# Kernel tuning notes

Hardware: AMD Instinct MI355X
Metric: run time of the kernel (lower is better)

Reference implementation:

```python
import jax, jax.numpy as jnp
import numpy as np

HIDDEN = 2048
N_HEADS = 32
N_KV_HEADS = 8
HEAD_DIM = HIDDEN // N_HEADS  # 64
N_REP = N_HEADS // N_KV_HEADS  # 4
ROPE_THETA = 10000.0


def setup_inputs() -> dict:
    key = jax.random.key(0)
    ks = jax.random.split(key, 5)
    b, s = 2, 2048
    x = jax.random.normal(ks[0], (b, s, HIDDEN), dtype=jnp.float32)
    position_ids = jnp.arange(b * s, dtype=jnp.int32).reshape(b, s)
    sc = 1.0 / np.sqrt(HIDDEN)
    Wq = jax.random.normal(ks[1], (HIDDEN, HIDDEN), dtype=jnp.float32) * sc
    Wk = jax.random.normal(ks[2], (HIDDEN, N_KV_HEADS * HEAD_DIM), dtype=jnp.float32) * sc
    Wv = jax.random.normal(ks[3], (HIDDEN, N_KV_HEADS * HEAD_DIM), dtype=jnp.float32) * sc
    Wo = jax.random.normal(ks[4], (HIDDEN, HIDDEN), dtype=jnp.float32) * sc
    return {"input_ids": x, "Wq": Wq, "Wk": Wk, "Wv": Wv, "Wo": Wo,
            "position_ids": position_ids}


def _rope_cos_sin(position_ids, dtype):
    # inv_freq: [head_dim/2]
    inv_freq = 1.0 / (ROPE_THETA ** (jnp.arange(0, HEAD_DIM, 2, dtype=jnp.float32) / HEAD_DIM))
    freqs = position_ids.astype(jnp.float32)[..., None] * inv_freq  # [b, s, d/2]
    emb = jnp.concatenate([freqs, freqs], axis=-1)  # [b, s, d]
    return emb.astype(dtype), None  # placeholder, replaced below


def _rotate_half(x):
    x1, x2 = jnp.split(x, 2, axis=-1)
    return jnp.concatenate([-x2, x1], axis=-1)


def reference(input_ids, Wq, Wk, Wv, Wo, position_ids):
    b, s, _ = input_ids.shape
    q = (input_ids @ Wq).reshape(b, s, N_HEADS, HEAD_DIM).transpose(0, 2, 1, 3)      # [b,H,s,d]
    k = (input_ids @ Wk).reshape(b, s, N_KV_HEADS, HEAD_DIM).transpose(0, 2, 1, 3)   # [b,Hkv,s,d]
    v = (input_ids @ Wv).reshape(b, s, N_KV_HEADS, HEAD_DIM).transpose(0, 2, 1, 3)

    # RoPE
    inv_freq = 1.0 / (ROPE_THETA ** (jnp.arange(0, HEAD_DIM, 2, dtype=jnp.float32) / HEAD_DIM))
    freqs = position_ids.astype(jnp.float32)[..., None] * inv_freq  # [b,s,d/2]
    emb = jnp.concatenate([freqs, freqs], axis=-1)                   # [b,s,d]
    cos = jnp.cos(emb).astype(input_ids.dtype)[:, None, :, :]        # [b,1,s,d]
    sin = jnp.sin(emb).astype(input_ids.dtype)[:, None, :, :]
    q = q * cos + _rotate_half(q) * sin
    k = k * cos + _rotate_half(k) * sin

    # repeat_kv: [b,Hkv,s,d] -> [b,H,s,d]
    k = jnp.repeat(k, N_REP, axis=1)
    v = jnp.repeat(v, N_REP, axis=1)

    # causal SDPA
    scale = 1.0 / np.sqrt(HEAD_DIM)
    scores = jnp.einsum('bhqd,bhkd->bhqk', q, k) * scale
    causal = jnp.tril(jnp.ones((s, s), dtype=bool))
    scores = jnp.where(causal, scores, jnp.finfo(scores.dtype).min)
    attn = jax.nn.softmax(scores, axis=-1)
    out = jnp.einsum('bhqk,bhkd->bhqd', attn, v)                     # [b,H,s,d]
    out = out.transpose(0, 2, 1, 3).reshape(b, s, HIDDEN)
    return out @ Wo
```

## Files before the change

### kernel.cpp

```cpp
#include <hip/hip_runtime.h>
#include <hip/hip_bf16.h>

#define HIDDEN 2048
#define NHEADS 32
#define NKVH   8
#define HD     64
#define BATCH  2
#define SEQ    2048
#define ROWS   (BATCH * SEQ)
#define NQKV   3072
#define KCOL   2048
#define VCOL   2560

typedef __bf16 bf16x8 __attribute__((ext_vector_type(8)));
typedef __bf16 bf16x4 __attribute__((ext_vector_type(4)));
typedef float  f32x4  __attribute__((ext_vector_type(4)));
typedef short  s16x4  __attribute__((ext_vector_type(4)));
typedef short  s16x8  __attribute__((ext_vector_type(8)));

__device__ __forceinline__ void gl2lds16(const void* g, void* l) {
  __builtin_amdgcn_global_load_lds(
      (const __attribute__((address_space(1))) void*)g,
      (__attribute__((address_space(3))) void*)l, 16, 0, 0);
}

__device__ __forceinline__ short f2bs(float f) {
  __bf16 h = (__bf16)f;
  return __builtin_bit_cast(short, h);
}

__device__ __forceinline__ float fexp2(float x) {
#if __has_builtin(__builtin_amdgcn_exp2f)
  return __builtin_amdgcn_exp2f(x);
#else
  return exp2f(x);
#endif
}

__device__ __forceinline__ f32x4 mfma16(s16x4 a, s16x4 b, f32x4 c) {
#if __has_builtin(__builtin_amdgcn_mfma_f32_16x16x16bf16_1k)
  return __builtin_amdgcn_mfma_f32_16x16x16bf16_1k(a, b, c, 0, 0, 0);
#else
  s16x8 a8 = __builtin_shufflevector(a, (s16x4){0,0,0,0}, 0,1,2,3,4,5,6,7);
  s16x8 b8 = __builtin_shufflevector(b, (s16x4){0,0,0,0}, 0,1,2,3,4,5,6,7);
  a8[4]=0;a8[5]=0;a8[6]=0;a8[7]=0; b8[4]=0;b8[5]=0;b8[6]=0;b8[7]=0;
  return __builtin_amdgcn_mfma_f32_16x16x32_bf16(
      __builtin_bit_cast(bf16x8, a8), __builtin_bit_cast(bf16x8, b8), c, 0, 0, 0);
#endif
}

__global__ void prep(const float* __restrict__ Wq, const float* __restrict__ Wk,
                     const float* __restrict__ Wv, const float* __restrict__ Wo,
                     const float* __restrict__ x,
                     __bf16* __restrict__ dstW, __bf16* __restrict__ Xb) {
  __shared__ __bf16 tile[32][33];
  int bid = blockIdx.x, tid = threadIdx.x;
  if (bid < 10240) {
    int n0 = (bid % 160) * 32, k0 = (bid / 160) * 32;
    int tx = tid & 31, ty = tid >> 5;
    const float* src;
    int N, c0;
    if (n0 < 2048)      { src = Wq; N = 2048; c0 = n0; }
    else if (n0 < 2560) { src = Wk; N = 512;  c0 = n0 - 2048; }
    else if (n0 < 3072) { src = Wv; N = 512;  c0 = n0 - 2560; }
    else                { src = Wo; N = 2048; c0 = n0 - 3072; }
#pragma unroll
    for (int i = 0; i < 32; i += 8)
      tile[ty + i][tx] = (__bf16)src[(size_t)(k0 + ty + i) * N + (c0 + tx)];
    __syncthreads();
#pragma unroll
    for (int i = 0; i < 32; i += 8)
      dstW[(size_t)(n0 + ty + i) * HIDDEN + (k0 + tx)] = tile[tx][ty + i];
  } else {
    size_t i = (size_t)(bid - 10240) * 256 + tid;
    const float4* s = (const float4*)(x + i * 16);
    float4 a = s[0], b = s[1], c = s[2], d = s[3];
    bf16x8 o0, o1;
    o0[0] = (__bf16)a.x; o0[1] = (__bf16)a.y; o0[2] = (__bf16)a.z; o0[3] = (__bf16)a.w;
    o0[4] = (__bf16)b.x; o0[5] = (__bf16)b.y; o0[6] = (__bf16)b.z; o0[7] = (__bf16)b.w;
    o1[0] = (__bf16)c.x; o1[1] = (__bf16)c.y; o1[2] = (__bf16)c.z; o1[3] = (__bf16)c.w;
    o1[4] = (__bf16)d.x; o1[5] = (__bf16)d.y; o1[6] = (__bf16)d.z; o1[7] = (__bf16)d.w;
    *(bf16x8*)(Xb + i * 16)     = o0;
    *(bf16x8*)(Xb + i * 16 + 8) = o1;
  }
}

template <typename OutT, bool ROPE>
__launch_bounds__(256, 2)
__global__ void gemm_bt(const __bf16* __restrict__ A, const __bf16* __restrict__ Bt,
                        OutT* __restrict__ C, int M, int N, int K,
                        const int* __restrict__ pos_ids, __bf16* __restrict__ Vt) {
  __shared__ __bf16 As[2][128 * 32];
  __shared__ __bf16 Bs[2][128 * 32];
  int id = blockIdx.x;
  int bm = (id & 7) * 4 + ((id >> 3) & 3);
  int bn = id >> 5;
  int t = threadIdx.x;
  int wave = t >> 6, lane = t & 63, l16 = lane & 15, quad = lane >> 4;
  int wm = (wave >> 1) * 64, wn = (wave & 1) * 64;

  f32x4 acc[4][4] = {};

  int arow = t >> 2;
  int ac   = (t & 3) * 8;
  const __bf16* Ag = A  + (size_t)(bm * 128 + arow) * K + ac;
  const __bf16* Bg = Bt + (size_t)(bn * 128 + arow) * K + ac;
  int woff = wave * 512;

  for (int k0 = 0; k0 < K; k0 += 64) {
    __syncthreads();
    gl2lds16(Ag + k0,                      &As[0][woff]);
    gl2lds16(Ag + (size_t)64 * K + k0,      &As[0][2048 + woff]);
    gl2lds16(Ag + k0 + 32,                 &As[1][woff]);
    gl2lds16(Ag + (size_t)64 * K + k0 + 32, &As[1][2048 + woff]);
    gl2lds16(Bg + k0,                      &Bs[0][woff]);
    gl2lds16(Bg + (size_t)64 * K + k0,      &Bs[0][2048 + woff]);
    gl2lds16(Bg + k0 + 32,                 &Bs[1][woff]);
    gl2lds16(Bg + (size_t)64 * K + k0 + 32, &Bs[1][2048 + woff]);
    __syncthreads();

#pragma unroll
    for (int ks = 0; ks < 2; ++ks) {
      bf16x8 af[4], bfr[4];
#pragma unroll
      for (int i = 0; i < 4; ++i) {
        af[i]  = *(const bf16x8*)(&As[ks][(wm + i * 16 + l16) * 32 + quad * 8]);
        bfr[i] = *(const bf16x8*)(&Bs[ks][(wn + i * 16 + l16) * 32 + quad * 8]);
      }
#pragma unroll
      for (int i = 0; i < 4; ++i)
#pragma unroll
        for (int j = 0; j < 4; ++j)
          acc[i][j] = __builtin_amdgcn_mfma_f32_16x16x32_bf16(af[i], bfr[j], acc[i][j], 0, 0, 0);
    }
  }

  if (ROPE) {
    int headidx = bn * 2 + (wn >> 6);
    if (headidx >= 40) {
#pragma unroll
      for (int i = 0; i < 4; ++i) {
        int srow = bm * 128 + wm + i * 16 + quad * 4;
        int b = srow >> 11, s = srow & 2047;
#pragma unroll
        for (int j = 0; j < 4; ++j) {
          int vcol = bn * 128 + wn + j * 16 + l16 - VCOL;
          int hk = vcol >> 6, d = vcol & 63;
          bf16x4 w;
#pragma unroll
          for (int r = 0; r < 4; ++r) w[r] = (__bf16)acc[i][j][r];
          *(bf16x4*)(Vt + ((size_t)(b * NKVH + hk) * HD + d) * SEQ + s) = w;
        }
      }
      return;
    }
    float invrev0 = __expf(-(float)l16 * 0.28782313662425574f) * 0.15915494309189535f;
    float invrev1 = __expf(-(float)(l16 + 16) * 0.28782313662425574f) * 0.15915494309189535f;
#pragma unroll
    for (int i = 0; i < 4; ++i)
#pragma unroll
      for (int r = 0; r < 4; ++r) {
        int gr = bm * 128 + wm + i * 16 + quad * 4 + r;
        float pos = (float)pos_ids[gr];
        float rv0 = pos * invrev0; rv0 -= floorf(rv0);
        float rv1 = pos * invrev1; rv1 -= floorf(rv1);
        float a0 = rv0 * 6.283185307179586f, a1 = rv1 * 6.283185307179586f;
        float s0 = __sinf(a0), c0 = __cosf(a0);
        float s1 = __sinf(a1), c1 = __cosf(a1);
        float x0 = acc[i][0][r], x2 = acc[i][2][r];
        acc[i][0][r] = x0 * c0 - x2 * s0;
        acc[i][2][r] = x2 * c0 + x0 * s0;
        float x1 = acc[i][1][r], x3 = acc[i][3][r];
        acc[i][1][r] = x1 * c1 - x3 * s1;
        acc[i][3][r] = x3 * c1 + x1 * s1;
      }
  }

#pragma unroll
  for (int i = 0; i < 4; ++i)
#pragma unroll
    for (int j = 0; j < 4; ++j)
#pragma unroll
      for (int r = 0; r < 4; ++r)
        C[(size_t)(bm * 128 + wm + i * 16 + quad * 4 + r) * N +
          (bn * 128 + wn + j * 16 + l16)] = (OutT)acc[i][j][r];
}

__launch_bounds__(256, 4)
__global__ void flash_attn(const __bf16* __restrict__ QKV, const __bf16* __restrict__ Vt,
                           __bf16* __restrict__ O) {
  int wgid = blockIdx.x + 64 * (blockIdx.y + 8 * (int)blockIdx.z);
  int swz  = (wgid & 7) * 128 + (wgid >> 3);
  int b  = swz >> 9;
  int hk = (swz >> 6) & 7;
  int bx = swz & 63;
  int p  = bx >> 2;
  int np = 31 - p;
  int h  = hk * 4 + (bx & 3);

  int t = threadIdx.x;
  int wave = t >> 6, lane = t & 63, l16 = lane & 15, quad = lane >> 4;

  __shared__ __bf16 Ks[2][2][64 * 32];
  __shared__ __bf16 Vs[2][4096];

  const __bf16* Kbase = QKV + (size_t)(b * SEQ) * NQKV + KCOL + hk * HD;
  const __bf16* VtB   = Vt + (size_t)(b * NKVH + hk) * HD * SEQ;

  int kr = wave * 16 + (lane >> 2);
  int kc = (lane & 3) * 8;
  int vd = wave * 16 + (lane >> 2);
  int vsc = (lane & 3) * 16;
  int vs4w = (lane & 3) * 4;

  const s16x4 vones = { (short)0x3F80, (short)0x3F80, (short)0x3F80, (short)0x3F80 };

  bf16x8 qfrag[2][2];
#pragma unroll
  for (int qi = 0; qi < 2; ++qi) {
    int qt = qi ? np : p;
    const __bf16* qp = QKV + (size_t)(b * SEQ + qt * 64 + wave * 16 + l16) * NQKV
                     + h * HD + quad * 8;
    bf16x8 q0 = *(const bf16x8*)qp;
    bf16x8 q1 = *(const bf16x8*)(qp + 32);
#pragma unroll
    for (int e = 0; e < 8; ++e) {
      qfrag[qi][0][e] = (__bf16)((float)q0[e] * 0.18033688011112042f);
      qfrag[qi][1][e] = (__bf16)((float)q1[e] * 0.18033688011112042f);
    }
  }

  f32x4 lacc[2] = { {0.f,0.f,0.f,0.f}, {0.f,0.f,0.f,0.f} };
  f32x4 oacc[2][4];
#pragma unroll
  for (int qi = 0; qi < 2; ++qi)
#pragma unroll
    for (int dt = 0; dt < 4; ++dt) oacc[qi][dt] = (f32x4){0.f, 0.f, 0.f, 0.f};

  {
    const __bf16* kp = Kbase + (size_t)kr * NQKV + kc;
    gl2lds16(kp,      &Ks[0][0][wave * 512]);
    gl2lds16(kp + 32, &Ks[0][1][wave * 512]);
    const __bf16* vp = VtB + (size_t)vd * SEQ + vsc;
    s16x8 v0 = __builtin_bit_cast(s16x8, *(const bf16x8*)vp);
    s16x8 v1 = __builtin_bit_cast(s16x8, *(const bf16x8*)(vp + 8));
    *(s16x4*)(&Vs[0][(vs4w + 0) * 256 + vd * 4]) = __builtin_shufflevector(v0, v0, 0, 1, 2, 3);
    *(s16x4*)(&Vs[0][(vs4w + 1) * 256 + vd * 4]) = __builtin_shufflevector(v0, v0, 4, 5, 6, 7);
    *(s16x4*)(&Vs[0][(vs4w + 2) * 256 + vd * 4]) = __builtin_shufflevector(v1, v1, 0, 1, 2, 3);
    *(s16x4*)(&Vs[0][(vs4w + 3) * 256 + vd * 4]) = __builtin_shufflevector(v1, v1, 4, 5, 6, 7);
  }

  for (int kt = 0; kt <= np; ++kt) {
    int buf = kt & 1;
    __syncthreads();

    bool pre = (kt < np);
    s16x8 pv0, pv1;
    if (pre) {
      const __bf16* kp = Kbase + (size_t)((kt + 1) * 64 + kr) * NQKV + kc;
      gl2lds16(kp,      &Ks[buf ^ 1][0][wave * 512]);
      gl2lds16(kp + 32, &Ks[buf ^ 1][1][wave * 512]);
      const __bf16* vp = VtB + (size_t)vd * SEQ + (kt + 1) * 64 + vsc;
      pv0 = __builtin_bit_cast(s16x8, *(const bf16x8*)vp);
      pv1 = __builtin_bit_cast(s16x8, *(const bf16x8*)(vp + 8));
    }

    bool a0 = (kt <= p);

    f32x4 s0[4], s1[4];
#pragma unroll
    for (int nt = 0; nt < 4; ++nt) {
      s0[nt] = (f32x4){0.f, 0.f, 0.f, 0.f};
      s1[nt] = (f32x4){0.f, 0.f, 0.f, 0.f};
    }
#pragma unroll
    for (int ks = 0; ks < 2; ++ks) {
      bf16x8 kf[4];
#pragma unroll
      for (int nt = 0; nt < 4; ++nt)
        kf[nt] = *(const bf16x8*)(&Ks[buf][ks][(nt * 16 + l16) * 32 + quad * 8]);
      __builtin_amdgcn_s_setprio(1);
#pragma unroll
      for (int nt = 0; nt < 4; ++nt)
        s1[nt] = __builtin_amdgcn_mfma_f32_16x16x32_bf16(kf[nt], qfrag[1][ks], s1[nt], 0, 0, 0);
      if (a0) {
#pragma unroll
        for (int nt = 0; nt < 4; ++nt)
          s0[nt] = __builtin_amdgcn_mfma_f32_16x16x32_bf16(kf[nt], qfrag[0][ks], s0[nt], 0, 0, 0);
      }
      __builtin_amdgcn_s_setprio(0);
    }

    s16x4 af0[4], af1[4];
    {
      int qg = wave * 16 + l16;
      if (kt == np) {
#pragma unroll
        for (int nt = 0; nt < 4; ++nt)
#pragma unroll
          for (int r = 0; r < 4; ++r) {
            int kg = nt * 16 + quad * 4 + r;
            af1[nt][r] = f2bs(fexp2((kg > qg) ? -1e30f : s1[nt][r]));
          }
      } else {
#pragma unroll
        for (int nt = 0; nt < 4; ++nt)
#pragma unroll
          for (int r = 0; r < 4; ++r)
            af1[nt][r] = f2bs(fexp2(s1[nt][r]));
      }
      if (a0) {
        if (kt == p) {
#pragma unroll
          for (int nt = 0; nt < 4; ++nt)
#pragma unroll
            for (int r = 0; r < 4; ++r) {
              int kg = nt * 16 + quad * 4 + r;
              af0[nt][r] = f2bs(fexp2((kg > qg) ? -1e30f : s0[nt][r]));
            }
        } else {
#pragma unroll
          for (int nt = 0; nt < 4; ++nt)
#pragma unroll
            for (int r = 0; r < 4; ++r)
              af0[nt][r] = f2bs(fexp2(s0[nt][r]));
        }
      }
    }

#pragma unroll
    for (int nt = 0; nt < 4; ++nt) {
      s16x4 vf[4];
#pragma unroll
      for (int dt = 0; dt < 4; ++dt)
        vf[dt] = *(const s16x4*)(&Vs[buf][(nt * 4 + quad) * 256 + (dt * 16 + l16) * 4]);
      __builtin_amdgcn_s_setprio(1);
#pragma unroll
      for (int dt = 0; dt < 4; ++dt)
        oacc[1][dt] = mfma16(af1[nt], vf[dt], oacc[1][dt]);
      lacc[1] = mfma16(af1[nt], vones, lacc[1]);
      if (a0) {
#pragma unroll
        for (int dt = 0; dt < 4; ++dt)
          oacc[0][dt] = mfma16(af0[nt], vf[dt], oacc[0][dt]);
        lacc[0] = mfma16(af0[nt], vones, lacc[0]);
      }
      __builtin_amdgcn_s_setprio(0);
    }

    if (pre) {
      *(s16x4*)(&Vs[buf ^ 1][(vs4w + 0) * 256 + vd * 4]) = __builtin_shufflevector(pv0, pv0, 0, 1, 2, 3);
      *(s16x4*)(&Vs[buf ^ 1][(vs4w + 1) * 256 + vd * 4]) = __builtin_shufflevector(pv0, pv0, 4, 5, 6, 7);
      *(s16x4*)(&Vs[buf ^ 1][(vs4w + 2) * 256 + vd * 4]) = __builtin_shufflevector(pv1, pv1, 0, 1, 2, 3);
      *(s16x4*)(&Vs[buf ^ 1][(vs4w + 3) * 256 + vd * 4]) = __builtin_shufflevector(pv1, pv1, 4, 5, 6, 7);
    }
  }

#pragma unroll
  for (int qi = 0; qi < 2; ++qi) {
    int qt = qi ? np : p;
#pragma unroll
    for (int r = 0; r < 4; ++r) {
      float inv = 1.0f / lacc[qi][r];
#pragma unroll
      for (int dt = 0; dt < 4; ++dt) {
        float o = oacc[qi][dt][r] * inv;
        O[(size_t)(b * SEQ + qt * 64 + wave * 16 + quad * 4 + r) * HIDDEN +
          h * HD + dt * 16 + l16] = (__bf16)o;
      }
    }
  }
}

extern "C" void kernel_launch(void* const* d_in, const int* in_sizes, int n_in,
                              void* d_out, int out_size, void* d_ws, size_t ws_size,
                              hipStream_t stream) {
  const float* x  = (const float*)d_in[0];
  const float* Wq = (const float*)d_in[1];
  const float* Wk = (const float*)d_in[2];
  const float* Wv = (const float*)d_in[3];
  const float* Wo = (const float*)d_in[4];
  const int* pos  = (const int*)d_in[5];

  __bf16* Wqkvt = (__bf16*)d_ws;
  __bf16* Wot   = Wqkvt + (size_t)NQKV * HIDDEN;
  __bf16* Xb    = Wot + (size_t)HIDDEN * HIDDEN;
  __bf16* QKV   = Xb + (size_t)ROWS * HIDDEN;
  __bf16* Oat   = QKV + (size_t)ROWS * NQKV;
  __bf16* Vt    = Xb;

  prep<<<dim3(12288), 256, 0, stream>>>(Wq, Wk, Wv, Wo, x, Wqkvt, Xb);

  gemm_bt<__bf16, true><<<dim3(768), 256, 0, stream>>>(
      Xb, Wqkvt, QKV, ROWS, NQKV, HIDDEN, pos, Vt);

  flash_attn<<<dim3(64, NKVH, BATCH), 256, 0, stream>>>(QKV, Vt, Oat);

  gemm_bt<float, false><<<dim3(512), 256, 0, stream>>>(
      Oat, Wot, (float*)d_out, ROWS, HIDDEN, HIDDEN, nullptr, nullptr);
}
```

Baseline: 285.9 us.

## Pair adjacent query tiles per workgroup with balanced XCD head mapping

```diff
diff --git a/kernel.cpp b/kernel.cpp
--- a/kernel.cpp
+++ b/kernel.cpp
@@ -190,13 +190,18 @@
 __global__ void flash_attn(const __bf16* __restrict__ QKV, const __bf16* __restrict__ Vt,
                            __bf16* __restrict__ O) {
   int wgid = blockIdx.x + 64 * (blockIdx.y + 8 * (int)blockIdx.z);
-  int swz  = (wgid & 7) * 128 + (wgid >> 3);
-  int b  = swz >> 9;
-  int hk = (swz >> 6) & 7;
-  int bx = swz & 63;
-  int p  = bx >> 2;
-  int np = 31 - p;
-  int h  = hk * 4 + (bx & 3);
+  int xcd  = wgid & 7;
+  int j    = wgid >> 3;
+  int G    = j >> 6;
+  int gid  = xcd * 2 + G;
+  int b    = gid >> 3;
+  int hk   = gid & 7;
+  int r    = j & 63;
+  int b0   = r & 1, b5 = (r >> 5) & 1;
+  int h    = hk * 4 + b0 + 2 * b5;
+  int M0   = (r >> 1) & 15;
+  int M    = (b0 ^ b5) ? (15 - M0) : M0;
+  int NT   = 2 * M + 2;
 
   int t = threadIdx.x;
   int wave = t >> 6, lane = t & 63, l16 = lane & 15, quad = lane >> 4;
@@ -209,7 +214,7 @@
 
   int kr = wave * 16 + (lane >> 2);
   int kc = (lane & 3) * 8;
-  int vd = wave * 16 + (lane >> 2);
+  int vd = kr;
   int vsc = (lane & 3) * 16;
   int vs4w = (lane & 3) * 4;
 
@@ -218,8 +223,7 @@
   bf16x8 qfrag[2][2];
 #pragma unroll
   for (int qi = 0; qi < 2; ++qi) {
-    int qt = qi ? np : p;
-    const __bf16* qp = QKV + (size_t)(b * SEQ + qt * 64 + wave * 16 + l16) * NQKV
+    const __bf16* qp = QKV + (size_t)(b * SEQ + M * 128 + qi * 64 + wave * 16 + l16) * NQKV
                      + h * HD + quad * 8;
     bf16x8 q0 = *(const bf16x8*)qp;
     bf16x8 q1 = *(const bf16x8*)(qp + 32);
@@ -250,11 +254,11 @@
     *(s16x4*)(&Vs[0][(vs4w + 3) * 256 + vd * 4]) = __builtin_shufflevector(v1, v1, 4, 5, 6, 7);
   }
 
-  for (int kt = 0; kt <= np; ++kt) {
+  for (int kt = 0; kt < NT; ++kt) {
     int buf = kt & 1;
     __syncthreads();
 
-    bool pre = (kt < np);
+    bool pre = (kt < NT - 1);
     s16x8 pv0, pv1;
     if (pre) {
       const __bf16* kp = Kbase + (size_t)((kt + 1) * 64 + kr) * NQKV + kc;
@@ -265,8 +269,6 @@
       pv1 = __builtin_bit_cast(s16x8, *(const bf16x8*)(vp + 8));
     }
 
-    bool a0 = (kt <= p);
-
     f32x4 s0[4], s1[4];
 #pragma unroll
     for (int nt = 0; nt < 4; ++nt) {
@@ -279,51 +281,49 @@
 #pragma unroll
       for (int nt = 0; nt < 4; ++nt)
         kf[nt] = *(const bf16x8*)(&Ks[buf][ks][(nt * 16 + l16) * 32 + quad * 8]);
-      __builtin_amdgcn_s_setprio(1);
 #pragma unroll
       for (int nt = 0; nt < 4; ++nt)
         s1[nt] = __builtin_amdgcn_mfma_f32_16x16x32_bf16(kf[nt], qfrag[1][ks], s1[nt], 0, 0, 0);
-      if (a0) {
+      if (pre) {
 #pragma unroll
         for (int nt = 0; nt < 4; ++nt)
           s0[nt] = __builtin_amdgcn_mfma_f32_16x16x32_bf16(kf[nt], qfrag[0][ks], s0[nt], 0, 0, 0);
       }
-      __builtin_amdgcn_s_setprio(0);
     }
 
     s16x4 af0[4], af1[4];
     {
       int qg = wave * 16 + l16;
-      if (kt == np) {
+      if (kt == NT - 1) {
 #pragma unroll
         for (int nt = 0; nt < 4; ++nt)
 #pragma unroll
-          for (int r = 0; r < 4; ++r) {
-            int kg = nt * 16 + quad * 4 + r;
-            af1[nt][r] = f2bs(fexp2((kg > qg) ? -1e30f : s1[nt][r]));
+          for (int rr = 0; rr < 4; ++rr) {
+            int kg = nt * 16 + quad * 4 + rr;
+            af1[nt][rr] = f2bs(fexp2((kg > qg) ? -1e30f : s1[nt][rr]));
           }
       } else {
 #pragma unroll
         for (int nt = 0; nt < 4; ++nt)
 #pragma unroll
-          for (int r = 0; r < 4; ++r)
-            af1[nt][r] = f2bs(fexp2(s1[nt][r]));
-      }
-      if (a0) {
-        if (kt == p) {
+          for (int rr = 0; rr < 4; ++rr)
+            af1[nt][rr] = f2bs(fexp2(s1[nt][rr]));
+      }
+      if (pre) {
+        if (kt == NT - 2) {
 #pragma unroll
           for (int nt = 0; nt < 4; ++nt)
 #pragma unroll
-            for (int r = 0; r < 4; ++r) {
-              int kg = nt * 16 + quad * 4 + r;
-              af0[nt][r] = f2bs(fexp2((kg > qg) ? -1e30f : s0[nt][r]));
+            for (int rr = 0; rr < 4; ++rr) {
+              int kg = nt * 16 + quad * 4 + rr;
+              af0[nt][rr] = f2bs(fexp2((kg > qg) ? -1e30f : s0[nt][rr]));
             }
         } else {
 #pragma unroll
           for (int nt = 0; nt < 4; ++nt)
 #pragma unroll
-            for (int r = 0; r < 4; ++r)
-              af0[nt][r] = f2bs(fexp2(s0[nt][r]));
+            for (int rr = 0; rr < 4; ++rr)
+              af0[nt][rr] = f2bs(fexp2(s0[nt][rr]));
         }
       }
     }
@@ -334,18 +334,16 @@
 #pragma unroll
       for (int dt = 0; dt < 4; ++dt)
         vf[dt] = *(const s16x4*)(&Vs[buf][(nt * 4 + quad) * 256 + (dt * 16 + l16) * 4]);
-      __builtin_amdgcn_s_setprio(1);
 #pragma unroll
       for (int dt = 0; dt < 4; ++dt)
         oacc[1][dt] = mfma16(af1[nt], vf[dt], oacc[1][dt]);
       lacc[1] = mfma16(af1[nt], vones, lacc[1]);
-      if (a0) {
+      if (pre) {
 #pragma unroll
         for (int dt = 0; dt < 4; ++dt)
           oacc[0][dt] = mfma16(af0[nt], vf[dt], oacc[0][dt]);
         lacc[0] = mfma16(af0[nt], vones, lacc[0]);
       }
-      __builtin_amdgcn_s_setprio(0);
     }
 
     if (pre) {
@@ -358,14 +356,13 @@
 
 #pragma unroll
   for (int qi = 0; qi < 2; ++qi) {
-    int qt = qi ? np : p;
-#pragma unroll
-    for (int r = 0; r < 4; ++r) {
-      float inv = 1.0f / lacc[qi][r];
+#pragma unroll
+    for (int rr = 0; rr < 4; ++rr) {
+      float inv = 1.0f / lacc[qi][rr];
 #pragma unroll
       for (int dt = 0; dt < 4; ++dt) {
-        float o = oacc[qi][dt][r] * inv;
-        O[(size_t)(b * SEQ + qt * 64 + wave * 16 + quad * 4 + r) * HIDDEN +
+        float o = oacc[qi][dt][rr] * inv;
+        O[(size_t)(b * SEQ + M * 128 + qi * 64 + wave * 16 + quad * 4 + rr) * HIDDEN +
           h * HD + dt * 16 + l16] = (__bf16)o;
       }
     }
```

New measurement: 273.8 us. -4.2%, faster.
